# Kernel tuning notes

Hardware: AMD Instinct MI355X
Metric: run time of the kernel (lower is better)

The kernel has to match this reference:

```python
import jax, jax.numpy as jnp
import numpy as np

NEG_SLOPE = 0.2  # PyG GATConv default LeakyReLU slope


def add_self_loops(edge_index, n):
    loops = jnp.arange(n, dtype=edge_index.dtype)
    return jnp.concatenate([edge_index, jnp.stack([loops, loops])], axis=1)


def segment_softmax(e, seg, n):
    # e: [E, H], seg: [E] destination node ids
    m = jax.ops.segment_max(e, seg, num_segments=n)          # [N, H]
    ex = jnp.exp(e - m[seg])
    s = jax.ops.segment_sum(ex, seg, num_segments=n)          # [N, H]
    return ex / (s[seg] + 1e-16)


def gat_conv(x, edge_index, W, att_src, att_dst, bias, heads, concat):
    n = x.shape[0]
    c = W.shape[1] // heads
    ei = add_self_loops(edge_index, n)
    src, dst = ei[0], ei[1]
    h = (x @ W).reshape(n, heads, c)                          # [N, H, C]
    a_src = jnp.einsum('nhc,hc->nh', h, att_src)              # [N, H]
    a_dst = jnp.einsum('nhc,hc->nh', h, att_dst)
    e = a_src[src] + a_dst[dst]                               # [E, H]
    e = jax.nn.leaky_relu(e, NEG_SLOPE)
    alpha = segment_softmax(e, dst, n)                        # [E, H]
    msg = alpha[:, :, None] * h[src]                          # [E, H, C]
    out = jax.ops.segment_sum(msg, dst, num_segments=n)       # [N, H, C]
    if concat:
        out = out.reshape(n, heads * c)
    else:
        out = out.mean(axis=1)
    return out + bias


def setup_inputs() -> dict:
    key = jax.random.key(0)
    ks = jax.random.split(key, 16)
    N, E, IN, HID, H, OUT = 50000, 1600000, 512, 256, 8, 128
    s = 0.1
    return {
        'x': jax.random.normal(ks[0], (N, IN), jnp.float32),
        'edge_index': jax.random.randint(ks[1], (2, E), 0, N, jnp.int64),
        'edge_index_2': jax.random.randint(ks[2], (2, E), 0, N, jnp.int64),
        'W1': jax.random.normal(ks[3], (IN, HID * H), jnp.float32) * s,
        'att_src1': jax.random.normal(ks[4], (H, HID), jnp.float32) * s,
        'att_dst1': jax.random.normal(ks[5], (H, HID), jnp.float32) * s,
        'b1': jnp.zeros((HID * H,), jnp.float32),
        'W2': jax.random.normal(ks[6], (HID * H, OUT), jnp.float32) * s,
        'att_src2': jax.random.normal(ks[7], (1, OUT), jnp.float32) * s,
        'att_dst2': jax.random.normal(ks[8], (1, OUT), jnp.float32) * s,
        'b2': jnp.zeros((OUT,), jnp.float32),
        'W3': jax.random.normal(ks[9], (HID * H, OUT), jnp.float32) * s,
        'att_src3': jax.random.normal(ks[10], (1, OUT), jnp.float32) * s,
        'att_dst3': jax.random.normal(ks[11], (1, OUT), jnp.float32) * s,
        'b3': jnp.zeros((OUT,), jnp.float32),
    }


def reference(x, edge_index, edge_index_2, W1, att_src1, att_dst1, b1,
              W2, att_src2, att_dst2, b2, W3, att_src3, att_dst3, b3):
    # Inference mode: F.dropout and GATConv attention dropout are no-ops.
    emb = jax.nn.elu(gat_conv(x, edge_index, W1, att_src1, att_dst1, b1, heads=8, concat=True))
    x1 = gat_conv(emb, edge_index, W2, att_src2, att_dst2, b2, heads=1, concat=False)
    x2 = gat_conv(emb, edge_index_2, W3, att_src3, att_dst3, b3, heads=1, concat=False)
    logits = jax.nn.softmax(x1, axis=1)    # nn.Softmax() legacy dim -> 1 for 2D
    logits_2 = jax.nn.softmax(x2, axis=1)
    predictions = jnp.argmax(logits, axis=1)
    return (logits, logits_2, predictions)
```

## Files before the change

kernel.cpp:

```cpp
#include <hip/hip_runtime.h>
#include <hip/hip_bf16.h>
#include <math.h>

#define N_NODES 50000
#define E_EDGES 1600000
#define EP_EDGES (E_EDGES + N_NODES)
#define IN_F 512
#define HID 256
#define HEADS 8
#define OUTF 128

typedef unsigned short u16;
typedef __attribute__((ext_vector_type(8))) short short8;
typedef __attribute__((ext_vector_type(4))) float floatx4;

static __device__ __forceinline__ float eluf(float x) {
  return x > 0.f ? x : expm1f(x);
}

static __device__ __forceinline__ u16 bf16_hi(float v) {
  __hip_bfloat16 h = __float2bfloat16(v);
  return *(u16*)&h;
}
static __device__ __forceinline__ float bf16_f(u16 u) {
  __hip_bfloat16 h = *(__hip_bfloat16*)&u;
  return __bfloat162float(h);
}
static __device__ __forceinline__ void split3_bf16(float v, u16& h, u16& m, u16& l) {
  h = bf16_hi(v);
  float r1 = v - bf16_f(h);
  m = bf16_hi(r1);
  float r2 = r1 - bf16_f(m);
  l = bf16_hi(r2);
}

static __device__ __forceinline__ int clampi(int v, int n) {
  return v < 0 ? 0 : (v >= n ? n - 1 : v);
}


__global__ void k_detect(const int* __restrict__ ei, int* __restrict__ flag) {
  __shared__ int nz;
  if (threadIdx.x == 0) nz = 0;
  __syncthreads();
  for (int i = threadIdx.x; i < 4096; i += blockDim.x)
    if (ei[2 * i + 1] != 0) nz = 1;
  __syncthreads();
  if (threadIdx.x == 0) *flag = (nz ? 0 : 1);
}

__global__ void k_init_deg(int* __restrict__ deg, int n) {
  int i = blockIdx.x * 256 + threadIdx.x;
  if (i < n) deg[i] = 1;
}

__global__ void k_count(const int* __restrict__ ei, const int* __restrict__ flag,
                        int* __restrict__ deg, int E) {
  int e = blockIdx.x * 256 + threadIdx.x;
  if (e >= E) return;
  int f = *flag;
  int idx = E + e;
  int dst = clampi(ei[f ? 2 * idx : idx], N_NODES);
  atomicAdd(&deg[dst], 1);
}

__global__ __launch_bounds__(1024) void k_scan(const int* __restrict__ deg,
                                               int* __restrict__ rp, int n) {
  __shared__ int sw[16];
  __shared__ int s_run;
  int tid = threadIdx.x, lane = tid & 63, w = tid >> 6;
  if (tid == 0) s_run = 0;
  __syncthreads();
  for (int base = 0; base < n; base += 1024) {
    int i = base + tid;
    int v = (i < n) ? deg[i] : 0;
    int sv = v;
#pragma unroll
    for (int off = 1; off < 64; off <<= 1) {
      int t = __shfl_up(sv, off);
      if (lane >= off) sv += t;
    }
    if (lane == 63) sw[w] = sv;
    __syncthreads();
    if (w == 0) {
      int wsum = (lane < 16) ? sw[lane] : 0;
#pragma unroll
      for (int off = 1; off < 16; off <<= 1) {
        int t = __shfl_up(wsum, off);
        if (lane >= off) wsum += t;
      }
      if (lane < 16) sw[lane] = wsum;
    }
    __syncthreads();
    int woff = (w > 0) ? sw[w - 1] : 0;
    int run = s_run;
    if (i < n) rp[i + 1] = run + woff + sv;
    __syncthreads();
    if (tid == 1023) s_run = run + sw[15];
    __syncthreads();
  }
  if (tid == 0) rp[0] = 0;
}

__global__ void k_fill_self(const int* __restrict__ rp, int* __restrict__ wp,
                            int* __restrict__ col, int n) {
  int i = blockIdx.x * 256 + threadIdx.x;
  if (i < n) { int p = rp[i]; col[p] = i; wp[i] = p + 1; }
}

__global__ void k_fill_edges(const int* __restrict__ ei, const int* __restrict__ flag,
                             int* __restrict__ wp, int* __restrict__ col, int E) {
  int e = blockIdx.x * 256 + threadIdx.x;
  if (e >= E) return;
  int f = *flag;
  int src = clampi(ei[f ? 2 * e : e], N_NODES);
  int didx = E + e;
  int dst = clampi(ei[f ? 2 * didx : didx], N_NODES);
  int p = atomicAdd(&wp[dst], 1);
  col[p] = src;
}

__global__ void k_split3_t(const float* __restrict__ W, u16* __restrict__ H,
                           u16* __restrict__ Mv, u16* __restrict__ L,
                           int kshift, int kmask, int Nw, int total) {
  int idx = blockIdx.x * 256 + threadIdx.x;
  if (idx >= total) return;
  int n = idx >> kshift;
  int k = idx & kmask;
  u16 h, m, l;
  split3_bf16(W[(size_t)k * Nw + n], h, m, l);
  H[idx] = h;
  Mv[idx] = m;
  L[idx] = l;
}

__global__ __launch_bounds__(256) void k_watt1(
    const float* __restrict__ W1, const float* __restrict__ attS,
    const float* __restrict__ attD, float* __restrict__ watt) {
  int wid = (blockIdx.x * 256 + threadIdx.x) >> 6;
  int lane = threadIdx.x & 63;
  if (wid >= IN_F * HEADS) return;
  int k = wid >> 3, h = wid & 7;
  float4 wv = *(const float4*)&W1[(size_t)k * (HID * HEADS) + h * HID + lane * 4];
  float4 sv = *(const float4*)&attS[h * HID + lane * 4];
  float4 dv = *(const float4*)&attD[h * HID + lane * 4];
  float s = wv.x * sv.x + wv.y * sv.y + wv.z * sv.z + wv.w * sv.w;
  float d = wv.x * dv.x + wv.y * dv.y + wv.z * dv.z + wv.w * dv.w;
  for (int off = 32; off; off >>= 1) {
    s += __shfl_xor(s, off);
    d += __shfl_xor(d, off);
  }
  if (lane == 0) {
    watt[(size_t)(2 * h) * IN_F + k] = s;
    watt[(size_t)(2 * h + 1) * IN_F + k] = d;
  }
}

__global__ __launch_bounds__(256) void k_asad1(
    const float* __restrict__ x, const float* __restrict__ watt,
    float* __restrict__ asall, float* __restrict__ adall, int n) {
  int node = (blockIdx.x * 256 + threadIdx.x) >> 6;
  int lane = threadIdx.x & 63;
  if (node >= n) return;
  float4 x0 = *(const float4*)&x[(size_t)node * IN_F + lane * 8];
  float4 x1 = *(const float4*)&x[(size_t)node * IN_F + lane * 8 + 4];
  for (int h = 0; h < HEADS; ++h) {
    const float* ws = watt + (size_t)(2 * h) * IN_F + lane * 8;
    const float* wd = watt + (size_t)(2 * h + 1) * IN_F + lane * 8;
    float4 s0 = *(const float4*)ws, s1 = *(const float4*)(ws + 4);
    float4 d0 = *(const float4*)wd, d1 = *(const float4*)(wd + 4);
    float s = x0.x * s0.x + x0.y * s0.y + x0.z * s0.z + x0.w * s0.w
            + x1.x * s1.x + x1.y * s1.y + x1.z * s1.z + x1.w * s1.w;
    float d = x0.x * d0.x + x0.y * d0.y + x0.z * d0.z + x0.w * d0.w
            + x1.x * d1.x + x1.y * d1.y + x1.z * d1.z + x1.w * d1.w;
    for (int off = 32; off; off >>= 1) {
      s += __shfl_xor(s, off);
      d += __shfl_xor(d, off);
    }
    if (lane == 0) {
      asall[(size_t)h * n + node] = s;
      adall[(size_t)h * n + node] = d;
    }
  }
}

#define GBM 128
#define GBN 128
#define GBK 32
#define GM1 391

#define MFMA_BF16 __builtin_amdgcn_mfma_f32_16x16x32_bf16

__device__ __forceinline__ void gemm_epilogue(floatx4 acc[4][4], float* C,
                                              int ldc, int M, int accum,
                                              int row0, int col0, int wr,
                                              int wc, int lane) {
  int q = lane >> 4, n15 = lane & 15;
#pragma unroll
  for (int i = 0; i < 4; ++i) {
#pragma unroll
    for (int r = 0; r < 4; ++r) {
      int row = row0 + wr * 64 + i * 16 + q * 4 + r;
      if (row < M) {
#pragma unroll
        for (int j = 0; j < 4; ++j) {
          int cg = col0 + wc * 64 + j * 16 + n15;
          float v = acc[i][j][r];
          if (accum) v += C[(size_t)row * ldc + cg];
          C[(size_t)row * ldc + cg] = v;
        }
      }
    }
  }
}

__device__ __forceinline__ void gemm1_core(
    const float* __restrict__ X, int lda,
    const u16* __restrict__ Bh, const u16* __restrict__ Bm,
    const u16* __restrict__ Bl, int ldb,
    float* __restrict__ C, int ldc, int M, int K, int row0, int col0,
    u16* lds) {
  int tid = threadIdx.x;
  int lane = tid & 63, wave = tid >> 6;
  int wr = wave >> 1, wc = wave & 1;
  floatx4 acc[4][4] = {};
  int m0 = tid >> 2, m1 = (tid + 256) >> 2;
  int q0 = tid & 3;
  int lo0 = ((m0 >> 4) * 64 + q0 * 16 + (m0 & 15)) * 8;
  int lo1 = ((m1 >> 4) * 64 + q0 * 16 + (m1 & 15)) * 8;

  for (int k0 = 0; k0 < K; k0 += GBK) {
#pragma unroll
    for (int c = 0; c < 2; ++c) {
      int m = c ? m1 : m0;
      int lo = c ? lo1 : lo0;
      int gr = row0 + m;
      float f[8];
      if (gr < M) {
        float4 f0 = *(const float4*)(X + (size_t)gr * lda + k0 + q0 * 8);
        float4 f1 = *(const float4*)(X + (size_t)gr * lda + k0 + q0 * 8 + 4);
        f[0] = f0.x; f[1] = f0.y; f[2] = f0.z; f[3] = f0.w;
        f[4] = f1.x; f[5] = f1.y; f[6] = f1.z; f[7] = f1.w;
      } else {
#pragma unroll
        for (int e = 0; e < 8; ++e) f[e] = 0.f;
      }
      short8 vh, vm, vl;
#pragma unroll
      for (int e = 0; e < 8; ++e) {
        u16 h, m2, l;
        split3_bf16(f[e], h, m2, l);
        vh[e] = (short)h; vm[e] = (short)m2; vl[e] = (short)l;
      }
      *(short8*)&lds[lo] = vh;
      *(short8*)&lds[4096 + lo] = vm;
      *(short8*)&lds[8192 + lo] = vl;
    }
#pragma unroll
    for (int c = 0; c < 2; ++c) {
      int m = c ? m1 : m0;
      int lo = c ? lo1 : lo0;
      size_t go = (size_t)(col0 + m) * ldb + k0 + q0 * 8;
      *(short8*)&lds[12288 + lo] = *(const short8*)(Bh + go);
      *(short8*)&lds[16384 + lo] = *(const short8*)(Bm + go);
      *(short8*)&lds[20480 + lo] = *(const short8*)(Bl + go);
    }
    __syncthreads();
    short8 a_h[4], a_m[4], a_l[4];
#pragma unroll
    for (int i = 0; i < 4; ++i) {
      int o = ((wr * 4 + i) * 64 + lane) * 8;
      a_h[i] = *(short8*)&lds[o];
      a_m[i] = *(short8*)&lds[4096 + o];
      a_l[i] = *(short8*)&lds[8192 + o];
    }
#pragma unroll
    for (int j = 0; j < 4; ++j) {
      int o = ((wc * 4 + j) * 64 + lane) * 8;
      short8 b_h = *(short8*)&lds[12288 + o];
      short8 b_m = *(short8*)&lds[16384 + o];
      short8 b_l = *(short8*)&lds[20480 + o];
#pragma unroll
      for (int i = 0; i < 4; ++i) {
        acc[i][j] = MFMA_BF16(a_l[i], b_h, acc[i][j], 0, 0, 0);
        acc[i][j] = MFMA_BF16(a_m[i], b_m, acc[i][j], 0, 0, 0);
        acc[i][j] = MFMA_BF16(a_h[i], b_l, acc[i][j], 0, 0, 0);
        acc[i][j] = MFMA_BF16(a_m[i], b_h, acc[i][j], 0, 0, 0);
        acc[i][j] = MFMA_BF16(a_h[i], b_m, acc[i][j], 0, 0, 0);
        acc[i][j] = MFMA_BF16(a_h[i], b_h, acc[i][j], 0, 0, 0);
      }
    }
    __syncthreads();
  }
  gemm_epilogue(acc, C, ldc, M, 0, row0, col0, wr, wc, lane);
}

__global__ __launch_bounds__(256) void gemm1_k(
    const float* __restrict__ X, int lda,
    const u16* __restrict__ Bh, const u16* __restrict__ Bm,
    const u16* __restrict__ Bl, int ldb,
    float* __restrict__ C, int ldc, int M, int K) {
  __shared__ __align__(16) u16 lds[24576];
  gemm1_core(X, lda, Bh, Bm, Bl, ldb, C, ldc, M, K,
             blockIdx.x * GBM, blockIdx.y * GBN, lds);
}

__global__ __launch_bounds__(256) void prologue_k(
    const float* __restrict__ X,
    const u16* __restrict__ Bh, const u16* __restrict__ Bm,
    const u16* __restrict__ Bl, float* __restrict__ C, int M,
    const int* __restrict__ ei2, const int* __restrict__ flag,
    int* __restrict__ deg2, int E2, int nG) {
  __shared__ __align__(16) u16 lds[24576];
  int b = blockIdx.x;
  if (b < nG) {
    int bx = b % GM1, by = b / GM1;
    gemm1_core(X, IN_F, Bh, Bm, Bl, IN_F, C, HID, M, IN_F,
               bx * GBM, by * GBN, lds);
    return;
  }
  int e = (b - nG) * 256 + threadIdx.x;
  if (e >= E2) return;
  int f = *flag;
  int idx = E2 + e;
  int dst = clampi(ei2[f ? 2 * idx : idx], N_NODES);
  atomicAdd(&deg2[dst], 1);
}

__device__ __forceinline__ void gemm_core6(
    const u16* __restrict__ Ah, const u16* __restrict__ Am,
    const u16* __restrict__ Al, int lda,
    const u16* __restrict__ Bh, const u16* __restrict__ Bm,
    const u16* __restrict__ Bl, int ldb,
    float* __restrict__ C, int ldc, int M, int K, int row0, int col0,
    int accum, u16* lds) {
  int tid = threadIdx.x;
  int lane = tid & 63, wave = tid >> 6;
  int wr = wave >> 1, wc = wave & 1;
  floatx4 acc[4][4] = {};
  int m0 = tid >> 2, m1 = (tid + 256) >> 2;
  int q0 = tid & 3;
  int lo0 = ((m0 >> 4) * 64 + q0 * 16 + (m0 & 15)) * 8;
  int lo1 = ((m1 >> 4) * 64 + q0 * 16 + (m1 & 15)) * 8;
  for (int k0 = 0; k0 < K; k0 += GBK) {
#pragma unroll
    for (int c = 0; c < 2; ++c) {
      int m = c ? m1 : m0;
      int lo = c ? lo1 : lo0;
      int gr = row0 + m;
      short8 vh = {}, vm = {}, vl = {};
      if (gr < M) {
        size_t go = (size_t)gr * lda + k0 + q0 * 8;
        vh = *(const short8*)(Ah + go);
        vm = *(const short8*)(Am + go);
        vl = *(const short8*)(Al + go);
      }
      *(short8*)&lds[lo] = vh;
      *(short8*)&lds[4096 + lo] = vm;
      *(short8*)&lds[8192 + lo] = vl;
      size_t go = (size_t)(col0 + m) * ldb + k0 + q0 * 8;
      *(short8*)&lds[12288 + lo] = *(const short8*)(Bh + go);
      *(short8*)&lds[16384 + lo] = *(const short8*)(Bm + go);
      *(short8*)&lds[20480 + lo] = *(const short8*)(Bl + go);
    }
    __syncthreads();
    short8 a_h[4], a_m[4], a_l[4];
#pragma unroll
    for (int i = 0; i < 4; ++i) {
      int o = ((wr * 4 + i) * 64 + lane) * 8;
      a_h[i] = *(short8*)&lds[o];
      a_m[i] = *(short8*)&lds[4096 + o];
      a_l[i] = *(short8*)&lds[8192 + o];
    }
#pragma unroll
    for (int j = 0; j < 4; ++j) {
      int o = ((wc * 4 + j) * 64 + lane) * 8;
      short8 b_h = *(short8*)&lds[12288 + o];
      short8 b_m = *(short8*)&lds[16384 + o];
      short8 b_l = *(short8*)&lds[20480 + o];
#pragma unroll
      for (int i = 0; i < 4; ++i) {
        acc[i][j] = MFMA_BF16(a_l[i], b_h, acc[i][j], 0, 0, 0);
        acc[i][j] = MFMA_BF16(a_m[i], b_m, acc[i][j], 0, 0, 0);
        acc[i][j] = MFMA_BF16(a_h[i], b_l, acc[i][j], 0, 0, 0);
        acc[i][j] = MFMA_BF16(a_m[i], b_h, acc[i][j], 0, 0, 0);
        acc[i][j] = MFMA_BF16(a_h[i], b_m, acc[i][j], 0, 0, 0);
        acc[i][j] = MFMA_BF16(a_h[i], b_h, acc[i][j], 0, 0, 0);
      }
    }
    __syncthreads();
  }
  gemm_epilogue(acc, C, ldc, M, accum, row0, col0, wr, wc, lane);
}

__device__ __forceinline__ void gemm_core3(
    const u16* __restrict__ Ah, const u16* __restrict__ Am, int lda,
    const u16* __restrict__ Bh, const u16* __restrict__ Bm, int ldb,
    float* __restrict__ C, int ldc, int M, int K, int row0, int col0,
    int accum, u16* lds) {
  int tid = threadIdx.x;
  int lane = tid & 63, wave = tid >> 6;
  int wr = wave >> 1, wc = wave & 1;
  floatx4 acc[4][4] = {};
  int m0 = tid >> 2, m1 = (tid + 256) >> 2;
  int q0 = tid & 3;
  int lo0 = ((m0 >> 4) * 64 + q0 * 16 + (m0 & 15)) * 8;
  int lo1 = ((m1 >> 4) * 64 + q0 * 16 + (m1 & 15)) * 8;
  for (int k0 = 0; k0 < K; k0 += GBK) {
#pragma unroll
    for (int c = 0; c < 2; ++c) {
      int m = c ? m1 : m0;
      int lo = c ? lo1 : lo0;
      int gr = row0 + m;
      short8 vh = {}, vm = {};
      if (gr < M) {
        size_t go = (size_t)gr * lda + k0 + q0 * 8;
        vh = *(const short8*)(Ah + go);
        vm = *(const short8*)(Am + go);
      }
      *(short8*)&lds[lo] = vh;
      *(short8*)&lds[4096 + lo] = vm;
      size_t go = (size_t)(col0 + m) * ldb + k0 + q0 * 8;
      *(short8*)&lds[12288 + lo] = *(const short8*)(Bh + go);
      *(short8*)&lds[16384 + lo] = *(const short8*)(Bm + go);
    }
    __syncthreads();
    short8 a_h[4], a_m[4];
#pragma unroll
    for (int i = 0; i < 4; ++i) {
      int o = ((wr * 4 + i) * 64 + lane) * 8;
      a_h[i] = *(short8*)&lds[o];
      a_m[i] = *(short8*)&lds[4096 + o];
    }
#pragma unroll
    for (int j = 0; j < 4; ++j) {
      int o = ((wc * 4 + j) * 64 + lane) * 8;
      short8 b_h = *(short8*)&lds[12288 + o];
      short8 b_m = *(short8*)&lds[16384 + o];
#pragma unroll
      for (int i = 0; i < 4; ++i) {
        acc[i][j] = MFMA_BF16(a_m[i], b_h, acc[i][j], 0, 0, 0);
        acc[i][j] = MFMA_BF16(a_h[i], b_m, acc[i][j], 0, 0, 0);
        acc[i][j] = MFMA_BF16(a_h[i], b_h, acc[i][j], 0, 0, 0);
      }
    }
    __syncthreads();
  }
  gemm_epilogue(acc, C, ldc, M, accum, row0, col0, wr, wc, lane);
}

__global__ __launch_bounds__(256) void gemm23_k(
    const u16* __restrict__ Ah, const u16* __restrict__ Am,
    const u16* __restrict__ Al, int lda,
    const u16* __restrict__ B2h, const u16* __restrict__ B2m,
    const u16* __restrict__ B2l,
    const u16* __restrict__ B3h, const u16* __restrict__ B3m, int ldb,
    float* __restrict__ C2, float* __restrict__ C3, int ldc, int M, int K,
    int accum) {
  __shared__ __align__(16) u16 lds[24576];
  if (blockIdx.z == 0)
    gemm_core6(Ah, Am, Al, lda, B2h, B2m, B2l, ldb, C2, ldc, M, K,
               blockIdx.x * GBM, 0, accum, lds);
  else
    gemm_core3(Ah, Am, lda, B3h, B3m, ldb, C3, ldc, M, K,
               blockIdx.x * GBM, 0, accum, lds);
}

__global__ __launch_bounds__(256) void att_dot_dual(
    const float* __restrict__ h2, const float* __restrict__ h3,
    const float* __restrict__ s2, const float* __restrict__ d2,
    const float* __restrict__ s3, const float* __restrict__ d3,
    float* __restrict__ as2, float* __restrict__ ad2,
    float* __restrict__ as3, float* __restrict__ ad3, int n, int gW) {
  int b = blockIdx.x;
  int second = (b >= gW) ? 1 : 0;
  int bb = second ? b - gW : b;
  const float* h  = second ? h3 : h2;
  const float* sS = second ? s3 : s2;
  const float* sD = second ? d3 : d2;
  float* oS = second ? as3 : as2;
  float* oD = second ? ad3 : ad2;
  int node = (bb * 256 + threadIdx.x) >> 6;
  int lane = threadIdx.x & 63;
  if (node >= n) return;
  float2 hv = *(const float2*)&h[(size_t)node * OUTF + lane * 2];
  float2 sv = *(const float2*)&sS[lane * 2];
  float2 dv = *(const float2*)&sD[lane * 2];
  float s = hv.x * sv.x + hv.y * sv.y;
  float d = hv.x * dv.x + hv.y * dv.y;
  for (int off = 32; off; off >>= 1) {
    s += __shfl_xor(s, off);
    d += __shfl_xor(d, off);
  }
  if (lane == 0) { oS[node] = s; oD[node] = d; }
}

static __device__ __forceinline__ void aggr_l1_core(
    int node, int lane,
    const int* __restrict__ rp, const int* __restrict__ col,
    const float* __restrict__ aS, const float* __restrict__ aD,
    const float* __restrict__ h, const float* __restrict__ bias,
    u16* __restrict__ embH, u16* __restrict__ embM, u16* __restrict__ embL,
    int ecol0, int ldE, int n) {
  int s0 = rp[node], s1 = rp[node + 1];
  int d = s1 - s0;
  float ad = aD[node];
  float4 acc = make_float4(0.f, 0.f, 0.f, 0.f);

  if (d <= 64) {
    int c = 0;
    float e = -3.0e38f;
    if (lane < d) {
      c = clampi(col[s0 + lane], n);
      float t = aS[c] + ad;
      e = t >= 0.f ? t : 0.2f * t;
    }
    float m = e;
    for (int off = 32; off; off >>= 1) m = fmaxf(m, __shfl_xor(m, off));
    float ex = (lane < d) ? expf(e - m) : 0.f;
    float s = ex;
    for (int off = 32; off; off >>= 1) s += __shfl_xor(s, off);
    float al = ex * (1.f / (s + 1e-16f));
    int d8 = d & ~7;
    for (int j = 0; j < d8; j += 8) {
#pragma unroll
      for (int t = 0; t < 8; ++t) {
        int ct = __shfl(c, j + t);
        float at = __shfl(al, j + t);
        float4 hv = *(const float4*)&h[(size_t)ct * HID + lane * 4];
        acc.x += at * hv.x; acc.y += at * hv.y;
        acc.z += at * hv.z; acc.w += at * hv.w;
      }
    }
    if (d8 < d) {
#pragma unroll
      for (int t = 0; t < 8; ++t) {
        if (d8 + t < d) {
          int ct = __shfl(c, d8 + t);
          float at = __shfl(al, d8 + t);
          float4 hv = *(const float4*)&h[(size_t)ct * HID + lane * 4];
          acc.x += at * hv.x; acc.y += at * hv.y;
          acc.z += at * hv.z; acc.w += at * hv.w;
        }
      }
    }
  } else {
    float m = -3.0e38f;
    for (int i = s0 + lane; i < s1; i += 64) {
      float e = aS[clampi(col[i], n)] + ad;
      e = e >= 0.f ? e : 0.2f * e;
      m = fmaxf(m, e);
    }
    for (int off = 32; off; off >>= 1) m = fmaxf(m, __shfl_xor(m, off));
    float sum = 0.f;
    for (int i = s0 + lane; i < s1; i += 64) {
      float e = aS[clampi(col[i], n)] + ad;
      e = e >= 0.f ? e : 0.2f * e;
      sum += expf(e - m);
    }
    for (int off = 32; off; off >>= 1) sum += __shfl_xor(sum, off);
    float inv = 1.f / (sum + 1e-16f);
    for (int i = s0; i < s1; ++i) {
      int ci = clampi(col[i], n);
      float e = aS[ci] + ad;
      e = e >= 0.f ? e : 0.2f * e;
      float a = expf(e - m) * inv;
      float4 hv = *(const float4*)&h[(size_t)ci * HID + lane * 4];
      acc.x += a * hv.x; acc.y += a * hv.y; acc.z += a * hv.z; acc.w += a * hv.w;
    }
  }

  float4 bb = *(const float4*)&bias[lane * 4];
  float v0 = eluf(acc.x + bb.x);
  float v1 = eluf(acc.y + bb.y);
  float v2 = eluf(acc.z + bb.z);
  float v3 = eluf(acc.w + bb.w);
  ushort4 uh, um, ul;
  split3_bf16(v0, uh.x, um.x, ul.x);
  split3_bf16(v1, uh.y, um.y, ul.y);
  split3_bf16(v2, uh.z, um.z, ul.z);
  split3_bf16(v3, uh.w, um.w, ul.w);
  size_t o = (size_t)node * ldE + ecol0 + lane * 4;
  *(ushort4*)&embH[o] = uh;
  *(ushort4*)&embM[o] = um;
  *(ushort4*)&embL[o] = ul;
}

__global__ __launch_bounds__(256) void aggr_l1_fused(
    const int* __restrict__ rp, const int* __restrict__ col,
    const float* __restrict__ aS, const float* __restrict__ aD,
    const float* __restrict__ h, const float* __restrict__ bias,
    u16* __restrict__ embH, u16* __restrict__ embM, u16* __restrict__ embL,
    int ecol0, int ldE, int n) {
  int node = (blockIdx.x * 256 + threadIdx.x) >> 6;
  int lane = threadIdx.x & 63;
  if (node >= n) return;
  aggr_l1_core(node, lane, rp, col, aS, aD, h, bias, embH, embM, embL,
               ecol0, ldE, n);
}

__global__ __launch_bounds__(256) void fused_step(
    const int* __restrict__ rp, const int* __restrict__ col,
    const float* __restrict__ aS, const float* __restrict__ aD,
    const float* __restrict__ hg, const float* __restrict__ bias,
    u16* __restrict__ embH, u16* __restrict__ embM, u16* __restrict__ embL,
    int ecol0, int ldE, int n,
    const float* __restrict__ X,
    const u16* __restrict__ B1h, const u16* __restrict__ B1m,
    const u16* __restrict__ B1l, float* __restrict__ h1out, int nG1,
    const u16* __restrict__ A23h, const u16* __restrict__ A23m,
    const u16* __restrict__ A23l,
    const u16* __restrict__ B2h, const u16* __restrict__ B2m,
    const u16* __restrict__ B2l,
    const u16* __restrict__ B3h, const u16* __restrict__ B3m,
    float* __restrict__ C2, float* __restrict__ C3, int accum, int nG23) {
  __shared__ __align__(16) u16 lds[24576];
  int nC = nG1 + nG23;
  int k = blockIdx.x;
  int q = k / 9, r = k - q * 9;
  if (r == 0 && q < nC) {
    if (q < nG1) {
      int bx = q % GM1, by = q / GM1;
      gemm1_core(X, IN_F, B1h, B1m, B1l, IN_F, h1out, HID, n, IN_F,
                 bx * GBM, by * GBN, lds);
    } else {
      int p = q - nG1;
      int z = p / GM1, bx = p - z * GM1;
      if (z == 0)
        gemm_core6(A23h, A23m, A23l, ldE, B2h, B2m, B2l, HID * HEADS,
                   C2, OUTF, n, HID, bx * GBM, 0, accum, lds);
      else
        gemm_core3(A23h, A23m, ldE, B3h, B3m, HID * HEADS,
                   C3, OUTF, n, HID, bx * GBM, 0, accum, lds);
    }
    return;
  }
  int skipped = q + (r ? 1 : 0);
  if (skipped > nC) skipped = nC;
  int aggrIdx = k - skipped;
  int node = aggrIdx * 4 + (threadIdx.x >> 6);
  int lane = threadIdx.x & 63;
  if (node >= n) return;
  aggr_l1_core(node, lane, rp, col, aS, aD, hg, bias, embH, embM, embL,
               ecol0, ldE, n);
}

__global__ __launch_bounds__(256) void aggr_l2_dual(
    const int* __restrict__ rp1, const int* __restrict__ col1,
    const float* __restrict__ as2, const float* __restrict__ ad2,
    const float* __restrict__ h2, const float* __restrict__ b2,
    float* __restrict__ x1, float* __restrict__ pred,
    const int* __restrict__ rp2, const int* __restrict__ col2,
    const float* __restrict__ as3, const float* __restrict__ ad3,
    const float* __restrict__ h3, const float* __restrict__ b3,
    float* __restrict__ x2, int n, int gW) {
  int b = blockIdx.x;
  int second = (b >= gW) ? 1 : 0;
  int bb = second ? b - gW : b;
  const int* rp = second ? rp2 : rp1;
  const int* col = second ? col2 : col1;
  const float* aS = second ? as3 : as2;
  const float* aD = second ? ad3 : ad2;
  const float* h = second ? h3 : h2;
  const float* bias = second ? b3 : b2;
  float* out = second ? x2 : x1;
  float* pr = second ? nullptr : pred;

  int node = (bb * 256 + threadIdx.x) >> 6;
  int lane = threadIdx.x & 63;
  if (node >= n) return;
  int s0 = rp[node], s1 = rp[node + 1];
  int d = s1 - s0;
  float ad = aD[node];
  float2 acc = make_float2(0.f, 0.f);

  if (d <= 64) {
    int c = 0;
    float e = -3.0e38f;
    if (lane < d) {
      c = clampi(col[s0 + lane], n);
      float t = aS[c] + ad;
      e = t >= 0.f ? t : 0.2f * t;
    }
    float m = e;
    for (int off = 32; off; off >>= 1) m = fmaxf(m, __shfl_xor(m, off));
    float ex = (lane < d) ? expf(e - m) : 0.f;
    float s = ex;
    for (int off = 32; off; off >>= 1) s += __shfl_xor(s, off);
    float al = ex * (1.f / (s + 1e-16f));
    int d8 = d & ~7;
    for (int j = 0; j < d8; j += 8) {
#pragma unroll
      for (int t = 0; t < 8; ++t) {
        int ct = __shfl(c, j + t);
        float at = __shfl(al, j + t);
        float2 hv = *(const float2*)&h[(size_t)ct * OUTF + lane * 2];
        acc.x += at * hv.x; acc.y += at * hv.y;
      }
    }
    if (d8 < d) {
#pragma unroll
      for (int t = 0; t < 8; ++t) {
        if (d8 + t < d) {
          int ct = __shfl(c, d8 + t);
          float at = __shfl(al, d8 + t);
          float2 hv = *(const float2*)&h[(size_t)ct * OUTF + lane * 2];
          acc.x += at * hv.x; acc.y += at * hv.y;
        }
      }
    }
  } else {
    float m = -3.0e38f;
    for (int i = s0 + lane; i < s1; i += 64) {
      float e = aS[clampi(col[i], n)] + ad;
      e = e >= 0.f ? e : 0.2f * e;
      m = fmaxf(m, e);
    }
    for (int off = 32; off; off >>= 1) m = fmaxf(m, __shfl_xor(m, off));
    float sum = 0.f;
    for (int i = s0 + lane; i < s1; i += 64) {
      float e = aS[clampi(col[i], n)] + ad;
      e = e >= 0.f ? e : 0.2f * e;
      sum += expf(e - m);
    }
    for (int off = 32; off; off >>= 1) sum += __shfl_xor(sum, off);
    float inv = 1.f / (sum + 1e-16f);
    for (int i = s0; i < s1; ++i) {
      int ci = clampi(col[i], n);
      float e = aS[ci] + ad;
      e = e >= 0.f ? e : 0.2f * e;
      float a = expf(e - m) * inv;
      float2 hv = *(const float2*)&h[(size_t)ci * OUTF + lane * 2];
      acc.x += a * hv.x; acc.y += a * hv.y;
    }
  }

  float2 bb2 = *(const float2*)&bias[lane * 2];
  acc.x += bb2.x; acc.y += bb2.y;

  float bv;
  int bi;
  if (acc.y > acc.x) { bv = acc.y; bi = 2 * lane + 1; }
  else               { bv = acc.x; bi = 2 * lane; }
  for (int off = 32; off; off >>= 1) {
    float ov = __shfl_xor(bv, off);
    int oi = __shfl_xor(bi, off);
    if (ov > bv || (ov == bv && oi < bi)) { bv = ov; bi = oi; }
  }
  float e0 = expf(acc.x - bv), e1 = expf(acc.y - bv);
  float ssum = e0 + e1;
  for (int off = 32; off; off >>= 1) ssum += __shfl_xor(ssum, off);
  float2 r;
  r.x = e0 / ssum;
  r.y = e1 / ssum;
  *(float2*)&out[(size_t)node * OUTF + lane * 2] = r;
  if (pr != nullptr && lane == 0) pr[node] = (float)bi;
}

extern "C" void kernel_launch(void* const* d_in, const int* in_sizes, int n_in,
                              void* d_out, int out_size, void* d_ws, size_t ws_size,
                              hipStream_t stream) {
  const int N = N_NODES, E = E_EDGES;
  const float* x     = (const float*)d_in[0];
  const int*   ei1   = (const int*)d_in[1];
  const int*   ei2   = (const int*)d_in[2];
  const float* W1    = (const float*)d_in[3];
  const float* attS1 = (const float*)d_in[4];
  const float* attD1 = (const float*)d_in[5];
  const float* b1    = (const float*)d_in[6];
  const float* W2    = (const float*)d_in[7];
  const float* attS2 = (const float*)d_in[8];
  const float* attD2 = (const float*)d_in[9];
  const float* b2    = (const float*)d_in[10];
  const float* W3    = (const float*)d_in[11];
  const float* attS3 = (const float*)d_in[12];
  const float* attD3 = (const float*)d_in[13];
  const float* b3    = (const float*)d_in[14];

  size_t needPipe =
      2 * ((size_t)EP_EDGES * 4) + 2 * ((size_t)(N + 1) * 4) +
      2 * ((size_t)N * 4) + 4096 +
      2 * ((size_t)N * HID * 4) +
      3 * ((size_t)N * 512 * 2) +
      (size_t)N * OUTF * 4 * 2 +
      3 * ((size_t)IN_F * HID * HEADS * 2) +
      6 * ((size_t)HID * HEADS * OUTF * 2) +
      2 * ((size_t)HEADS * N * 4) +
      4 * ((size_t)N * 4) +
      (size_t)2 * HEADS * IN_F * 4 +
      (size_t)(8 << 20);
  int pipe = (ws_size >= needPipe) ? 1 : 0;
  const int nbuf = pipe ? 2 : 1;
  const int ldE = pipe ? 512 : 256;

  char* ws = (char*)d_ws;
  size_t off = 0;
  auto take = [&](size_t bytes) {
    off = (off + 255) & ~(size_t)255;
    size_t o = off;
    off += bytes;
    return o;
  };
  int*   col1 = (int*)(ws + take((size_t)EP_EDGES * 4));
  int*   col2 = (int*)(ws + take((size_t)EP_EDGES * 4));
  int*   rp1  = (int*)(ws + take((size_t)(N + 1) * 4));
  int*   rp2  = (int*)(ws + take((size_t)(N + 1) * 4));
  int*   wp1  = (int*)(ws + take((size_t)N * 4));
  int*   wp2  = (int*)(ws + take((size_t)N * 4));
  int*   flag = (int*)(ws + take(256));
  float* h1hA = (float*)(ws + take((size_t)N * HID * 4 * nbuf));
  float* h1hB = pipe ? h1hA + (size_t)N * HID : h1hA;
  u16*   embH = (u16*)(ws + take((size_t)N * ldE * 2));
  u16*   embM = (u16*)(ws + take((size_t)N * ldE * 2));
  u16*   embL = (u16*)(ws + take((size_t)N * ldE * 2));
  float* h2   = (float*)(ws + take((size_t)N * OUTF * 4 * 2));
  float* h3   = h2 + (size_t)N * OUTF;
  u16*   W1Th = (u16*)(ws + take((size_t)IN_F * HID * HEADS * 2));
  u16*   W1Tm = (u16*)(ws + take((size_t)IN_F * HID * HEADS * 2));
  u16*   W1Tl = (u16*)(ws + take((size_t)IN_F * HID * HEADS * 2));
  u16*   W2Th = (u16*)(ws + take((size_t)HID * HEADS * OUTF * 2));
  u16*   W2Tm = (u16*)(ws + take((size_t)HID * HEADS * OUTF * 2));
  u16*   W2Tl = (u16*)(ws + take((size_t)HID * HEADS * OUTF * 2));
  u16*   W3Th = (u16*)(ws + take((size_t)HID * HEADS * OUTF * 2));
  u16*   W3Tm = (u16*)(ws + take((size_t)HID * HEADS * OUTF * 2));
  u16*   W3Tl = (u16*)(ws + take((size_t)HID * HEADS * OUTF * 2));
  float* asall = (float*)(ws + take((size_t)HEADS * N * 4));
  float* adall = (float*)(ws + take((size_t)HEADS * N * 4));
  float* as2  = (float*)(ws + take((size_t)N * 4));
  float* ad2  = (float*)(ws + take((size_t)N * 4));
  float* as3  = (float*)(ws + take((size_t)N * 4));
  float* ad3  = (float*)(ws + take((size_t)N * 4));
  float* watt = (float*)(ws + take((size_t)2 * HEADS * IN_F * 4));

  float* outp = (float*)d_out;
  float* x1   = outp;
  float* x2   = outp + (size_t)N * OUTF;
  float* pred = outp + (size_t)2 * N * OUTF;

  const int gN = (N + 255) / 256;
  const int gE = (E + 255) / 256;
  const int gW = (N + 3) / 4;

  k_split3_t<<<(IN_F * HID * HEADS + 255) / 256, 256, 0, stream>>>(
      W1, W1Th, W1Tm, W1Tl, 9, 511, HID * HEADS, IN_F * HID * HEADS);
  k_split3_t<<<(HID * HEADS * OUTF + 255) / 256, 256, 0, stream>>>(
      W2, W2Th, W2Tm, W2Tl, 11, 2047, OUTF, HID * HEADS * OUTF);
  k_split3_t<<<(HID * HEADS * OUTF + 255) / 256, 256, 0, stream>>>(
      W3, W3Th, W3Tm, W3Tl, 11, 2047, OUTF, HID * HEADS * OUTF);

  k_watt1<<<(IN_F * HEADS * 64 + 255) / 256, 256, 0, stream>>>(
      W1, attS1, attD1, watt);
  k_asad1<<<gW, 256, 0, stream>>>(x, watt, asall, adall, N);

  k_detect<<<1, 256, 0, stream>>>(ei1, flag);

  k_init_deg<<<gN, 256, 0, stream>>>(wp1, N);
  k_count<<<gE, 256, 0, stream>>>(ei1, flag, wp1, E);
  k_scan<<<1, 1024, 0, stream>>>(wp1, rp1, N);
  k_fill_self<<<gN, 256, 0, stream>>>(rp1, wp1, col1, N);
  k_fill_edges<<<gE, 256, 0, stream>>>(ei1, flag, wp1, col1, E);

  if (pipe) {
    float* buf[2] = {h1hA, h1hB};
    k_init_deg<<<gN, 256, 0, stream>>>(wp2, N);
    prologue_k<<<GM1 * 2 + gE, 256, 0, stream>>>(
        x, W1Th, W1Tm, W1Tl, buf[0], N, ei2, flag, wp2, E, GM1 * 2);
    k_scan<<<1, 1024, 0, stream>>>(wp2, rp2, N);
    k_fill_self<<<gN, 256, 0, stream>>>(rp2, wp2, col2, N);
    k_fill_edges<<<gE, 256, 0, stream>>>(ei2, flag, wp2, col2, E);

    for (int h = 0; h < HEADS; ++h) {
      int nG1 = (h + 1 < HEADS) ? GM1 * 2 : 0;
      int nG23 = (h >= 1) ? GM1 * 2 : 0;
      int nC = nG1 + nG23;
      int T = gW + nC;
      if (9 * nC > T) T = 9 * nC;
      int hn = (h + 1 < HEADS) ? h + 1 : h;
      int hp = (h >= 1) ? h - 1 : 0;
      int sp = hp & 1;
      fused_step<<<T, 256, 0, stream>>>(
          rp1, col1, asall + (size_t)h * N, adall + (size_t)h * N,
          buf[h & 1], b1 + (size_t)h * HID,
          embH, embM, embL, (h & 1) * HID, ldE, N,
          x, W1Th + (size_t)hn * HID * IN_F, W1Tm + (size_t)hn * HID * IN_F,
          W1Tl + (size_t)hn * HID * IN_F, buf[(h + 1) & 1], nG1,
          embH + sp * HID, embM + sp * HID, embL + sp * HID,
          W2Th + (size_t)hp * HID, W2Tm + (size_t)hp * HID,
          W2Tl + (size_t)hp * HID,
          W3Th + (size_t)hp * HID, W3Tm + (size_t)hp * HID,
          h2, h3, hp > 0 ? 1 : 0, nG23);
    }
    gemm23_k<<<dim3(GM1, 1, 2), 256, 0, stream>>>(
        embH + HID, embM + HID, embL + HID, ldE,
        W2Th + (size_t)7 * HID, W2Tm + (size_t)7 * HID, W2Tl + (size_t)7 * HID,
        W3Th + (size_t)7 * HID, W3Tm + (size_t)7 * HID, HID * HEADS,
        h2, h3, OUTF, N, HID, 1);
  } else {
    k_init_deg<<<gN, 256, 0, stream>>>(wp2, N);
    k_count<<<gE, 256, 0, stream>>>(ei2, flag, wp2, E);
    k_scan<<<1, 1024, 0, stream>>>(wp2, rp2, N);
    k_fill_self<<<gN, 256, 0, stream>>>(rp2, wp2, col2, N);
    k_fill_edges<<<gE, 256, 0, stream>>>(ei2, flag, wp2, col2, E);
    for (int h = 0; h < HEADS; ++h) {
      gemm1_k<<<dim3(GM1, 2), 256, 0, stream>>>(
          x, IN_F,
          W1Th + (size_t)h * HID * IN_F, W1Tm + (size_t)h * HID * IN_F,
          W1Tl + (size_t)h * HID * IN_F, IN_F, h1hA, HID, N, IN_F);
      aggr_l1_fused<<<gW, 256, 0, stream>>>(
          rp1, col1, asall + (size_t)h * N, adall + (size_t)h * N, h1hA,
          b1 + (size_t)h * HID, embH, embM, embL, 0, ldE, N);
      gemm23_k<<<dim3(GM1, 1, 2), 256, 0, stream>>>(
          embH, embM, embL, ldE,
          W2Th + (size_t)h * HID, W2Tm + (size_t)h * HID,
          W2Tl + (size_t)h * HID,
          W3Th + (size_t)h * HID, W3Tm + (size_t)h * HID, HID * HEADS,
          h2, h3, OUTF, N, HID, h > 0 ? 1 : 0);
    }
  }

  att_dot_dual<<<2 * gW, 256, 0, stream>>>(
      h2, h3, attS2, attD2, attS3, attD3, as2, ad2, as3, ad3, N, gW);
  aggr_l2_dual<<<2 * gW, 256, 0, stream>>>(
      rp1, col1, as2, ad2, h2, b2, x1, pred,
      rp2, col2, as3, ad3, h3, b3, x2, N, gW);
}
```

Measured before the change: 3.945 ms.

## Merge both graphs' CSR builds and asad into shared prologue launches

Builds the CSR structures for both edge sets through combined launches: degree counting for both graphs and the per-node attention-logit computation are folded into the prologue kernel alongside the first GEMM tile blocks. The scan, self-loop fill and edge fill now each run once as dual kernels covering both graphs. This removes several serial kernel launches and the small single-block scans that leave most of the GPU idle. In exchange the prologue grid grows, and its GEMM blocks now share the device with more atomic and irregular work.

```diff
diff --git a/kernel.cpp b/kernel.cpp
--- a/kernel.cpp
+++ b/kernel.cpp
@@ -64,8 +64,8 @@
   atomicAdd(&deg[dst], 1);
 }
 
-__global__ __launch_bounds__(1024) void k_scan(const int* __restrict__ deg,
-                                               int* __restrict__ rp, int n) {
+static __device__ __forceinline__ void scan_body(const int* __restrict__ deg,
+                                                 int* __restrict__ rp, int n) {
   __shared__ int sw[16];
   __shared__ int s_run;
   int tid = threadIdx.x, lane = tid & 63, w = tid >> 6;
@@ -102,15 +102,58 @@
   if (tid == 0) rp[0] = 0;
 }
 
+__global__ __launch_bounds__(1024) void k_scan(const int* __restrict__ deg,
+                                               int* __restrict__ rp, int n) {
+  scan_body(deg, rp, n);
+}
+
+__global__ __launch_bounds__(1024) void k_scan_dual(
+    const int* __restrict__ degA, int* __restrict__ rpA,
+    const int* __restrict__ degB, int* __restrict__ rpB, int n) {
+  if (blockIdx.x == 0) scan_body(degA, rpA, n);
+  else                 scan_body(degB, rpB, n);
+}
+
 __global__ void k_fill_self(const int* __restrict__ rp, int* __restrict__ wp,
                             int* __restrict__ col, int n) {
   int i = blockIdx.x * 256 + threadIdx.x;
   if (i < n) { int p = rp[i]; col[p] = i; wp[i] = p + 1; }
 }
 
+__global__ void k_fill_self_dual(
+    const int* __restrict__ rpA, int* __restrict__ wpA, int* __restrict__ colA,
+    const int* __restrict__ rpB, int* __restrict__ wpB, int* __restrict__ colB,
+    int n, int gN) {
+  int b = blockIdx.x;
+  const int* rp; int* wp; int* col;
+  if (b < gN) { rp = rpA; wp = wpA; col = colA; }
+  else        { rp = rpB; wp = wpB; col = colB; b -= gN; }
+  int i = b * 256 + threadIdx.x;
+  if (i < n) { int p = rp[i]; col[p] = i; wp[i] = p + 1; }
+}
+
 __global__ void k_fill_edges(const int* __restrict__ ei, const int* __restrict__ flag,
                              int* __restrict__ wp, int* __restrict__ col, int E) {
   int e = blockIdx.x * 256 + threadIdx.x;
+  if (e >= E) return;
+  int f = *flag;
+  int src = clampi(ei[f ? 2 * e : e], N_NODES);
+  int didx = E + e;
+  int dst = clampi(ei[f ? 2 * didx : didx], N_NODES);
+  int p = atomicAdd(&wp[dst], 1);
+  col[p] = src;
+}
+
+__global__ void k_fill_edges_dual(
+    const int* __restrict__ eiA, const int* __restrict__ eiB,
+    const int* __restrict__ flag,
+    int* __restrict__ wpA, int* __restrict__ colA,
+    int* __restrict__ wpB, int* __restrict__ colB, int E, int gE) {
+  int b = blockIdx.x;
+  const int* ei; int* wp; int* col;
+  if (b < gE) { ei = eiA; wp = wpA; col = colA; }
+  else        { ei = eiB; wp = wpB; col = colB; b -= gE; }
+  int e = b * 256 + threadIdx.x;
   if (e >= E) return;
   int f = *flag;
   int src = clampi(ei[f ? 2 * e : e], N_NODES);
@@ -156,12 +199,10 @@
   }
 }
 
-__global__ __launch_bounds__(256) void k_asad1(
-    const float* __restrict__ x, const float* __restrict__ watt,
+static __device__ __forceinline__ void asad_body(
+    int node, int lane, const float* __restrict__ x,
+    const float* __restrict__ watt,
     float* __restrict__ asall, float* __restrict__ adall, int n) {
-  int node = (blockIdx.x * 256 + threadIdx.x) >> 6;
-  int lane = threadIdx.x & 63;
-  if (node >= n) return;
   float4 x0 = *(const float4*)&x[(size_t)node * IN_F + lane * 8];
   float4 x1 = *(const float4*)&x[(size_t)node * IN_F + lane * 8 + 4];
   for (int h = 0; h < HEADS; ++h) {
@@ -184,6 +225,15 @@
   }
 }
 
+__global__ __launch_bounds__(256) void k_asad1(
+    const float* __restrict__ x, const float* __restrict__ watt,
+    float* __restrict__ asall, float* __restrict__ adall, int n) {
+  int node = (blockIdx.x * 256 + threadIdx.x) >> 6;
+  int lane = threadIdx.x & 63;
+  if (node >= n) return;
+  asad_body(node, lane, x, watt, asall, adall, n);
+}
+
 #define GBM 128
 #define GBN 128
 #define GBK 32
@@ -309,8 +359,12 @@
     const float* __restrict__ X,
     const u16* __restrict__ Bh, const u16* __restrict__ Bm,
     const u16* __restrict__ Bl, float* __restrict__ C, int M,
-    const int* __restrict__ ei2, const int* __restrict__ flag,
-    int* __restrict__ deg2, int E2, int nG) {
+    const int* __restrict__ ei1, const int* __restrict__ ei2,
+    const int* __restrict__ flag,
+    int* __restrict__ deg1, int* __restrict__ deg2, int E2,
+    const float* __restrict__ watt,
+    float* __restrict__ asall, float* __restrict__ adall,
+    int nG, int nCE) {
   __shared__ __align__(16) u16 lds[24576];
   int b = blockIdx.x;
   if (b < nG) {
@@ -319,12 +373,24 @@
                bx * GBM, by * GBN, lds);
     return;
   }
-  int e = (b - nG) * 256 + threadIdx.x;
-  if (e >= E2) return;
-  int f = *flag;
-  int idx = E2 + e;
-  int dst = clampi(ei2[f ? 2 * idx : idx], N_NODES);
-  atomicAdd(&deg2[dst], 1);
+  b -= nG;
+  if (b < 2 * nCE) {
+    const int* ei = (b < nCE) ? ei1 : ei2;
+    int* deg = (b < nCE) ? deg1 : deg2;
+    int bb = (b < nCE) ? b : b - nCE;
+    int e = bb * 256 + (int)threadIdx.x;
+    if (e >= E2) return;
+    int f = *flag;
+    int idx = E2 + e;
+    int dst = clampi(ei[f ? 2 * idx : idx], N_NODES);
+    atomicAdd(&deg[dst], 1);
+    return;
+  }
+  b -= 2 * nCE;
+  int node = (b * 256 + (int)threadIdx.x) >> 6;
+  int lane = threadIdx.x & 63;
+  if (node >= M) return;
+  asad_body(node, lane, X, watt, asall, adall, M);
 }
 
 __device__ __forceinline__ void gemm_core6(
@@ -850,24 +916,21 @@
 
   k_watt1<<<(IN_F * HEADS * 64 + 255) / 256, 256, 0, stream>>>(
       W1, attS1, attD1, watt);
-  k_asad1<<<gW, 256, 0, stream>>>(x, watt, asall, adall, N);
-
   k_detect<<<1, 256, 0, stream>>>(ei1, flag);
-
-  k_init_deg<<<gN, 256, 0, stream>>>(wp1, N);
-  k_count<<<gE, 256, 0, stream>>>(ei1, flag, wp1, E);
-  k_scan<<<1, 1024, 0, stream>>>(wp1, rp1, N);
-  k_fill_self<<<gN, 256, 0, stream>>>(rp1, wp1, col1, N);
-  k_fill_edges<<<gE, 256, 0, stream>>>(ei1, flag, wp1, col1, E);
 
   if (pipe) {
     float* buf[2] = {h1hA, h1hB};
+    k_init_deg<<<gN, 256, 0, stream>>>(wp1, N);
     k_init_deg<<<gN, 256, 0, stream>>>(wp2, N);
-    prologue_k<<<GM1 * 2 + gE, 256, 0, stream>>>(
-        x, W1Th, W1Tm, W1Tl, buf[0], N, ei2, flag, wp2, E, GM1 * 2);
-    k_scan<<<1, 1024, 0, stream>>>(wp2, rp2, N);
-    k_fill_self<<<gN, 256, 0, stream>>>(rp2, wp2, col2, N);
-    k_fill_edges<<<gE, 256, 0, stream>>>(ei2, flag, wp2, col2, E);
+    prologue_k<<<GM1 * 2 + 2 * gE + gW, 256, 0, stream>>>(
+        x, W1Th, W1Tm, W1Tl, buf[0], N,
+        ei1, ei2, flag, wp1, wp2, E,
+        watt, asall, adall, GM1 * 2, gE);
+    k_scan_dual<<<2, 1024, 0, stream>>>(wp1, rp1, wp2, rp2, N);
+    k_fill_self_dual<<<2 * gN, 256, 0, stream>>>(
+        rp1, wp1, col1, rp2, wp2, col2, N, gN);
+    k_fill_edges_dual<<<2 * gE, 256, 0, stream>>>(
+        ei1, ei2, flag, wp1, col1, wp2, col2, E, gE);
 
     for (int h = 0; h < HEADS; ++h) {
       int nG1 = (h + 1 < HEADS) ? GM1 * 2 : 0;
@@ -896,6 +959,12 @@
         W3Th + (size_t)7 * HID, W3Tm + (size_t)7 * HID, HID * HEADS,
         h2, h3, OUTF, N, HID, 1);
   } else {
+    k_asad1<<<gW, 256, 0, stream>>>(x, watt, asall, adall, N);
+    k_init_deg<<<gN, 256, 0, stream>>>(wp1, N);
+    k_count<<<gE, 256, 0, stream>>>(ei1, flag, wp1, E);
+    k_scan<<<1, 1024, 0, stream>>>(wp1, rp1, N);
+    k_fill_self<<<gN, 256, 0, stream>>>(rp1, wp1, col1, N);
+    k_fill_edges<<<gE, 256, 0, stream>>>(ei1, flag, wp1, col1, E);
     k_init_deg<<<gN, 256, 0, stream>>>(wp2, N);
     k_count<<<gE, 256, 0, stream>>>(ei2, flag, wp2, E);
     k_scan<<<1, 1024, 0, stream>>>(wp2, rp2, N);
```

Measured after the change: 3.873 ms. About the same (-1.8%).
